# Kernel tuning notes

Hardware: AMD Instinct MI355X
Metric: run time of the kernel (lower is better)

Reference implementation:

```python
import jax, jax.numpy as jnp
import numpy as np

HID = 256

def setup_inputs() -> dict:
    key = jax.random.key(0)
    ks = jax.random.split(key, 16)
    B, N, DIN, DOUT = 256, 1024, 64, 128
    def lin(k, fin, fout):
        kw, kb = jax.random.split(k)
        s = 1.0 / np.sqrt(fin)
        W = jax.random.uniform(kw, (fin, fout), jnp.float32, -s, s)
        b = jax.random.uniform(kb, (fout,), jnp.float32, -s, s)
        return W, b
    x = jax.random.normal(ks[0], (B, N, DIN), jnp.float32)
    mask = jax.random.randint(ks[1], (B, N), 0, 2) > 0
    pw1, pb1 = lin(ks[2], DIN, HID)
    pw2, pb2 = lin(ks[3], HID, HID)
    pw3, pb3 = lin(ks[4], HID, HID)
    rw1, rb1 = lin(ks[5], HID, HID)
    rw2, rb2 = lin(ks[6], HID, HID)
    rw3, rb3 = lin(ks[7], HID, DOUT)
    return dict(x=x, mask=mask, pw1=pw1, pb1=pb1, pw2=pw2, pb2=pb2, pw3=pw3, pb3=pb3,
                rw1=rw1, rb1=rb1, rw2=rw2, rb2=rb2, rw3=rw3, rb3=rb3)

def reference(x, mask, pw1, pb1, pw2, pb2, pw3, pb3, rw1, rb1, rw2, rb2, rw3, rb3):
    # x: [B, N, din], mask: [B, N] bool
    # phi per element (padding elements are zeroed before the pool, matching
    # the torch pack/pad pipeline which only runs phi on valid elements)
    h = jax.nn.relu(jnp.einsum('bnd,dh->bnh', x, pw1) + pb1)
    h = jax.nn.relu(jnp.einsum('bnh,hk->bnk', h, pw2) + pb2)
    h = jnp.einsum('bnh,hk->bnk', h, pw3) + pb3
    m = mask.astype(x.dtype)[..., None]                  # [B, N, 1]
    pooled = jnp.sum(h * m, axis=1)                      # [B, 256]
    o = jax.nn.relu(pooled @ rw1 + rb1)
    o = jax.nn.relu(o @ rw2 + rb2)
    o = o @ rw3 + rb3                                    # [B, dout]
    # rows with zero valid elements get exactly 0 (torch leaves res at 0.0)
    valid = jnp.any(mask, axis=1, keepdims=True)
    return jnp.where(valid, o, jnp.zeros((), dtype=o.dtype))
```

## Files before the change

kernel.cpp:

```cpp
#include <hip/hip_runtime.h>

namespace {
constexpr int NB = 256, NN = 1024, DIN = 64, HID = 256, DOUT = 128;
constexpr int MT = 64;

typedef __attribute__((ext_vector_type(8))) short bf16x8;
typedef __attribute__((ext_vector_type(4))) float f32x4;

__device__ inline unsigned short f2bf(float f) {
    union { float f; unsigned u; } v; v.f = f;
    unsigned r = v.u + 0x7FFF + ((v.u >> 16) & 1);
    return (unsigned short)(r >> 16);
}

__device__ inline float4 dotseg(const float* __restrict__ buf, const float* __restrict__ W,
                                int c, int s) {
    const float4* W4 = (const float4*)W;
    float4 acc = make_float4(0.f, 0.f, 0.f, 0.f);
#pragma unroll 8
    for (int i = 0; i < 32; ++i) {
        int k = s * 32 + i;
        float bk = buf[k];
        float4 w = W4[(size_t)k * 64 + c];
        acc.x = fmaf(bk, w.x, acc.x);
        acc.y = fmaf(bk, w.y, acc.y);
        acc.z = fmaf(bk, w.z, acc.z);
        acc.w = fmaf(bk, w.w, acc.w);
    }
    return acc;
}

__launch_bounds__(512, 1)
__global__ void deepset(const float* __restrict__ x, const int* __restrict__ mask,
                        const float* __restrict__ pw1, const float* __restrict__ pb1,
                        const float* __restrict__ pw2, const float* __restrict__ pb2,
                        const float* __restrict__ pw3, const float* __restrict__ pb3,
                        const float* __restrict__ rw1, const float* __restrict__ rb1,
                        const float* __restrict__ rw2, const float* __restrict__ rb2,
                        const float* __restrict__ rw3, const float* __restrict__ rb3,
                        float* __restrict__ out)
{
    __shared__ unsigned short xs[2][MT * 64];
    __shared__ unsigned short h1s[2][MT * 256];
    __shared__ short vlist[NN];
    __shared__ float pooledS[HID];
    __shared__ float part[8][HID];
    __shared__ float bufB[HID], bufC[HID];
    __shared__ int cnt_s;

    const int b = blockIdx.x, t = threadIdx.x;
    const int lane = t & 63, wq = t >> 6;
    const int quad = lane >> 4, l15 = lane & 15;

    if (t == 0) cnt_s = 0;
    __syncthreads();
#pragma unroll
    for (int h = 0; h < 2; ++h) {
        int idx = h * 512 + t;
        int m = mask[b * NN + idx] != 0;
        unsigned long long bal = __ballot(m);
        int pos = __popcll(bal & ((1ULL << lane) - 1ULL));
        int wbase = 0;
        if (lane == 0) wbase = atomicAdd(&cnt_s, (int)__popcll(bal));
        wbase = __shfl(wbase, 0, 64);
        if (m) vlist[wbase + pos] = (short)idx;
    }

    uint4 w1f[2][2], w2f[8][2];
    float bias1[2], bias2[2];
#pragma unroll
    for (int j = 0; j < 2; ++j) {
        const int col = wq * 32 + j * 16 + l15;
        bias1[j] = pb1[col]; bias2[j] = pb2[col];
#pragma unroll
        for (int kk = 0; kk < 2; ++kk) {
            unsigned short tmp[8];
#pragma unroll
            for (int jj = 0; jj < 8; ++jj)
                tmp[jj] = f2bf(pw1[(size_t)(kk * 32 + quad * 8 + jj) * HID + col]);
            w1f[kk][j] = *(const uint4*)tmp;
        }
#pragma unroll
        for (int kk = 0; kk < 8; ++kk) {
            unsigned short tmp[8];
#pragma unroll
            for (int jj = 0; jj < 8; ++jj)
                tmp[jj] = f2bf(pw2[(size_t)(kk * 32 + quad * 8 + jj) * HID + col]);
            w2f[kk][j] = *(const uint4*)tmp;
        }
    }

    __syncthreads();
    const int cnt = cnt_s;
    const int T = (cnt + MT - 1) / MT;

    float pool[2] = {0.f, 0.f};
    const float* xb = x + (size_t)b * NN * DIN;
    const int gr = t >> 3, seg8 = t & 7;
    const int xoff = gr * 64 + ((seg8 ^ (gr & 7)) << 3);

    if (T > 0) {
        float4 a0 = make_float4(0.f,0.f,0.f,0.f), a1 = a0;
        if (gr < min(MT, cnt)) {
            const float4* p = (const float4*)(xb + (size_t)vlist[gr] * DIN + seg8 * 8);
            a0 = p[0]; a1 = p[1];
        }
        unsigned short tmp[8] = {f2bf(a0.x),f2bf(a0.y),f2bf(a0.z),f2bf(a0.w),
                                 f2bf(a1.x),f2bf(a1.y),f2bf(a1.z),f2bf(a1.w)};
        *(uint4*)&xs[0][xoff] = *(const uint4*)tmp;
    }

    int p = 0;
    for (int i = 0; i <= T; ++i, p ^= 1) {
        __syncthreads();
        const bool doL1 = (i < T);
        const bool hn = ((i + 1) * MT) < cnt;

        float4 n0 = make_float4(0.f,0.f,0.f,0.f), n1 = n0;
        if (doL1 && gr < cnt - (i + 1) * MT) {
            const float4* pp = (const float4*)(xb + (size_t)vlist[(i + 1) * MT + gr] * DIN + seg8 * 8);
            n0 = pp[0]; n1 = pp[1];
        }

        if (doL1) {
            f32x4 acc[4][2];
#pragma unroll
            for (int f = 0; f < 4; ++f)
#pragma unroll
                for (int j = 0; j < 2; ++j) acc[f][j] = (f32x4){0.f,0.f,0.f,0.f};
#pragma unroll
            for (int kk = 0; kk < 2; ++kk) {
                bf16x8 a[4];
#pragma unroll
                for (int f = 0; f < 4; ++f)
                    a[f] = *(const bf16x8*)&xs[p][(f*16 + l15)*64 + (((kk*4 + quad) ^ (l15 & 7)) << 3)];
#pragma unroll
                for (int j = 0; j < 2; ++j) {
                    bf16x8 bw = __builtin_bit_cast(bf16x8, w1f[kk][j]);
#pragma unroll
                    for (int f = 0; f < 4; ++f)
                        acc[f][j] = __builtin_amdgcn_mfma_f32_16x16x32_bf16(a[f], bw, acc[f][j], 0, 0, 0);
                }
            }
#pragma unroll
            for (int f = 0; f < 4; ++f)
#pragma unroll
                for (int j = 0; j < 2; ++j) {
                    int col = wq * 32 + j * 16 + l15, kb = col >> 3, cl = col & 7;
#pragma unroll
                    for (int r = 0; r < 4; ++r) {
                        int row = f * 16 + quad * 4 + r;
                        float h = fmaxf(acc[f][j][r] + bias1[j], 0.f);
                        h1s[p][row * 256 + ((kb ^ (row & 7)) << 3) + cl] = f2bf(h);
                    }
                }
        }

        if (i > 0) {
            const int basep = (i - 1) * MT;
            f32x4 acc2[4][2];
#pragma unroll
            for (int f = 0; f < 4; ++f)
#pragma unroll
                for (int j = 0; j < 2; ++j) acc2[f][j] = (f32x4){0.f,0.f,0.f,0.f};
#pragma unroll
            for (int kk = 0; kk < 8; ++kk) {
                bf16x8 a[4];
#pragma unroll
                for (int f = 0; f < 4; ++f)
                    a[f] = *(const bf16x8*)&h1s[p ^ 1][(f*16 + l15)*256 + (((kk*4 + quad) ^ (l15 & 7)) << 3)];
#pragma unroll
                for (int j = 0; j < 2; ++j) {
                    bf16x8 bw = __builtin_bit_cast(bf16x8, w2f[kk][j]);
#pragma unroll
                    for (int f = 0; f < 4; ++f)
                        acc2[f][j] = __builtin_amdgcn_mfma_f32_16x16x32_bf16(a[f], bw, acc2[f][j], 0, 0, 0);
                }
            }
#pragma unroll
            for (int f = 0; f < 4; ++f)
#pragma unroll
                for (int r = 0; r < 4; ++r) {
                    bool v = (basep + f * 16 + quad * 4 + r) < cnt;
#pragma unroll
                    for (int j = 0; j < 2; ++j) {
                        float h = fmaxf(acc2[f][j][r] + bias2[j], 0.f);
                        pool[j] += v ? h : 0.f;
                    }
                }
        }

        if (hn) {
            unsigned short tmp[8] = {f2bf(n0.x),f2bf(n0.y),f2bf(n0.z),f2bf(n0.w),
                                     f2bf(n1.x),f2bf(n1.y),f2bf(n1.z),f2bf(n1.w)};
            *(uint4*)&xs[p ^ 1][xoff] = *(const uint4*)tmp;
        }
    }

#pragma unroll
    for (int j = 0; j < 2; ++j) {
        float v = pool[j];
        v += __shfl_xor(v, 16, 64);
        v += __shfl_xor(v, 32, 64);
        if (quad == 0) pooledS[wq * 32 + j * 16 + l15] = v;
    }
    __syncthreads();

    const int c = t & 63, s = t >> 6;
    {
        float4 pt = dotseg(pooledS, pw3, c, s);
        ((float4*)part[s])[c] = pt;
        __syncthreads();
        if (t < HID) {
            float v = (float)cnt * pb3[t];
#pragma unroll
            for (int g = 0; g < 8; ++g) v += part[g][t];
            bufB[t] = v;
        }
        __syncthreads();
    }
    {
        float4 pt = dotseg(bufB, rw1, c, s);
        ((float4*)part[s])[c] = pt;
        __syncthreads();
        if (t < HID) {
            float v = rb1[t];
#pragma unroll
            for (int g = 0; g < 8; ++g) v += part[g][t];
            bufC[t] = fmaxf(v, 0.f);
        }
        __syncthreads();
    }
    {
        float4 pt = dotseg(bufC, rw2, c, s);
        ((float4*)part[s])[c] = pt;
        __syncthreads();
        if (t < HID) {
            float v = rb2[t];
#pragma unroll
            for (int g = 0; g < 8; ++g) v += part[g][t];
            bufB[t] = fmaxf(v, 0.f);
        }
        __syncthreads();
    }
    {
        const int c4 = t & 31, s4 = t >> 5;
        const float4* W4 = (const float4*)rw3;
        float4 acc = make_float4(0.f, 0.f, 0.f, 0.f);
#pragma unroll 8
        for (int i = 0; i < 16; ++i) {
            int k = s4 * 16 + i;
            float bk = bufB[k];
            float4 w = W4[(size_t)k * 32 + c4];
            acc.x = fmaf(bk, w.x, acc.x);
            acc.y = fmaf(bk, w.y, acc.y);
            acc.z = fmaf(bk, w.z, acc.z);
            acc.w = fmaf(bk, w.w, acc.w);
        }
        float* part2 = &part[0][0];
        ((float4*)(part2 + s4 * DOUT))[c4] = acc;
        __syncthreads();
        if (t < DOUT) {
            float v = rb3[t];
#pragma unroll
            for (int g = 0; g < 16; ++g) v += part2[g * DOUT + t];
            out[b * DOUT + t] = (cnt > 0) ? v : 0.f;
        }
    }
}
}

extern "C" void kernel_launch(void* const* d_in, const int* in_sizes, int n_in,
                              void* d_out, int out_size, void* d_ws, size_t ws_size,
                              hipStream_t stream) {
    const float* x    = (const float*)d_in[0];
    const int*   mask = (const int*)  d_in[1];
    const float* pw1  = (const float*)d_in[2];
    const float* pb1  = (const float*)d_in[3];
    const float* pw2  = (const float*)d_in[4];
    const float* pb2  = (const float*)d_in[5];
    const float* pw3  = (const float*)d_in[6];
    const float* pb3  = (const float*)d_in[7];
    const float* rw1  = (const float*)d_in[8];
    const float* rb1  = (const float*)d_in[9];
    const float* rw2  = (const float*)d_in[10];
    const float* rb2  = (const float*)d_in[11];
    const float* rw3  = (const float*)d_in[12];
    const float* rb3  = (const float*)d_in[13];
    float* out = (float*)d_out;
    (void)d_ws; (void)ws_size;

    deepset<<<dim3(NB), dim3(512), 0, stream>>>(x, mask, pw1, pb1, pw2, pb2,
                                                pw3, pb3, rw1, rb1, rw2, rb2, rw3, rb3, out);
}
```

Baseline: 147.7 us.

## Swap MFMA operands for transposed output and interleave layer-1/layer-2 MFMAs

Swaps the A/B operands of the MFMA calls so each lane holds 4 consecutive hidden columns for one row. This allows packed 8-byte bf16 stores of the layer-1 activations into LDS, and float4 bias loads, in place of scalar 2-byte stores. It also merges the layer-1 and layer-2 MFMA loops into one k-loop so the independent MFMAs interleave, and changes the pooling reduction to shuffles across the 16 lanes. The cost is more live accumulator registers at once, which may raise register pressure.

```diff
diff --git a/kernel.cpp b/kernel.cpp
--- a/kernel.cpp
+++ b/kernel.cpp
@@ -51,6 +51,8 @@
     const int b = blockIdx.x, t = threadIdx.x;
     const int lane = t & 63, wq = t >> 6;
     const int quad = lane >> 4, l15 = lane & 15;
+    const int sw = l15 & 7;
+    const int cb0 = wq * 32 + quad * 4;
 
     if (t == 0) cnt_s = 0;
     __syncthreads();
@@ -67,11 +69,12 @@
     }
 
     uint4 w1f[2][2], w2f[8][2];
-    float bias1[2], bias2[2];
+    float4 bias1v[2], bias2v[2];
 #pragma unroll
     for (int j = 0; j < 2; ++j) {
         const int col = wq * 32 + j * 16 + l15;
-        bias1[j] = pb1[col]; bias2[j] = pb2[col];
+        bias1v[j] = *(const float4*)&pb1[cb0 + j * 16];
+        bias2v[j] = *(const float4*)&pb2[cb0 + j * 16];
 #pragma unroll
         for (int kk = 0; kk < 2; ++kk) {
             unsigned short tmp[8];
@@ -94,7 +97,7 @@
     const int cnt = cnt_s;
     const int T = (cnt + MT - 1) / MT;
 
-    float pool[2] = {0.f, 0.f};
+    float pool[2][4] = {{0.f,0.f,0.f,0.f},{0.f,0.f,0.f,0.f}};
     const float* xb = x + (size_t)b * NN * DIN;
     const int gr = t >> 3, seg8 = t & 7;
     const int xoff = gr * 64 + ((seg8 ^ (gr & 7)) << 3);
@@ -114,6 +117,7 @@
     for (int i = 0; i <= T; ++i, p ^= 1) {
         __syncthreads();
         const bool doL1 = (i < T);
+        const bool doL2 = (i > 0);
         const bool hn = ((i + 1) * MT) < cnt;
 
         float4 n0 = make_float4(0.f,0.f,0.f,0.f), n1 = n0;
@@ -122,71 +126,77 @@
             n0 = pp[0]; n1 = pp[1];
         }
 
-        if (doL1) {
-            f32x4 acc[4][2];
-#pragma unroll
-            for (int f = 0; f < 4; ++f)
-#pragma unroll
-                for (int j = 0; j < 2; ++j) acc[f][j] = (f32x4){0.f,0.f,0.f,0.f};
-#pragma unroll
-            for (int kk = 0; kk < 2; ++kk) {
-                bf16x8 a[4];
+        f32x4 acc[2][4], acc2[2][4];
+#pragma unroll
+        for (int j = 0; j < 2; ++j)
+#pragma unroll
+            for (int f = 0; f < 4; ++f) {
+                acc[j][f]  = (f32x4){0.f,0.f,0.f,0.f};
+                acc2[j][f] = (f32x4){0.f,0.f,0.f,0.f};
+            }
+
+#pragma unroll
+        for (int kk = 0; kk < 8; ++kk) {
+            bf16x8 aL2[4], aL1[4];
+            if (doL2) {
 #pragma unroll
                 for (int f = 0; f < 4; ++f)
-                    a[f] = *(const bf16x8*)&xs[p][(f*16 + l15)*64 + (((kk*4 + quad) ^ (l15 & 7)) << 3)];
+                    aL2[f] = *(const bf16x8*)&h1s[p ^ 1][(f*16 + l15)*256 + (((kk*4 + quad) ^ sw) << 3)];
+            }
+            if (doL1 && kk < 2) {
+#pragma unroll
+                for (int f = 0; f < 4; ++f)
+                    aL1[f] = *(const bf16x8*)&xs[p][(f*16 + l15)*64 + (((kk*4 + quad) ^ sw) << 3)];
 #pragma unroll
                 for (int j = 0; j < 2; ++j) {
                     bf16x8 bw = __builtin_bit_cast(bf16x8, w1f[kk][j]);
 #pragma unroll
                     for (int f = 0; f < 4; ++f)
-                        acc[f][j] = __builtin_amdgcn_mfma_f32_16x16x32_bf16(a[f], bw, acc[f][j], 0, 0, 0);
+                        acc[j][f] = __builtin_amdgcn_mfma_f32_16x16x32_bf16(bw, aL1[f], acc[j][f], 0, 0, 0);
                 }
             }
-#pragma unroll
-            for (int f = 0; f < 4; ++f)
+            if (doL2) {
 #pragma unroll
                 for (int j = 0; j < 2; ++j) {
-                    int col = wq * 32 + j * 16 + l15, kb = col >> 3, cl = col & 7;
-#pragma unroll
-                    for (int r = 0; r < 4; ++r) {
-                        int row = f * 16 + quad * 4 + r;
-                        float h = fmaxf(acc[f][j][r] + bias1[j], 0.f);
-                        h1s[p][row * 256 + ((kb ^ (row & 7)) << 3) + cl] = f2bf(h);
-                    }
+                    bf16x8 bw2 = __builtin_bit_cast(bf16x8, w2f[kk][j]);
+#pragma unroll
+                    for (int f = 0; f < 4; ++f)
+                        acc2[j][f] = __builtin_amdgcn_mfma_f32_16x16x32_bf16(bw2, aL2[f], acc2[j][f], 0, 0, 0);
                 }
-        }
-
-        if (i > 0) {
+            }
+        }
+
+        if (doL1) {
+#pragma unroll
+            for (int j = 0; j < 2; ++j) {
+                int kb = wq * 4 + j * 2 + (quad >> 1);
+#pragma unroll
+                for (int f = 0; f < 4; ++f) {
+                    int row = f * 16 + l15;
+                    unsigned lo = (unsigned)f2bf(fmaxf(acc[j][f][0] + bias1v[j].x, 0.f))
+                                | ((unsigned)f2bf(fmaxf(acc[j][f][1] + bias1v[j].y, 0.f)) << 16);
+                    unsigned hi = (unsigned)f2bf(fmaxf(acc[j][f][2] + bias1v[j].z, 0.f))
+                                | ((unsigned)f2bf(fmaxf(acc[j][f][3] + bias1v[j].w, 0.f)) << 16);
+                    *(uint2*)&h1s[p][row * 256 + ((kb ^ sw) << 3) + ((quad & 1) << 2)] = make_uint2(lo, hi);
+                }
+            }
+        }
+
+        if (doL2) {
             const int basep = (i - 1) * MT;
-            f32x4 acc2[4][2];
-#pragma unroll
-            for (int f = 0; f < 4; ++f)
-#pragma unroll
-                for (int j = 0; j < 2; ++j) acc2[f][j] = (f32x4){0.f,0.f,0.f,0.f};
-#pragma unroll
-            for (int kk = 0; kk < 8; ++kk) {
-                bf16x8 a[4];
-#pragma unroll
-                for (int f = 0; f < 4; ++f)
-                    a[f] = *(const bf16x8*)&h1s[p ^ 1][(f*16 + l15)*256 + (((kk*4 + quad) ^ (l15 & 7)) << 3)];
-#pragma unroll
-                for (int j = 0; j < 2; ++j) {
-                    bf16x8 bw = __builtin_bit_cast(bf16x8, w2f[kk][j]);
-#pragma unroll
-                    for (int f = 0; f < 4; ++f)
-                        acc2[f][j] = __builtin_amdgcn_mfma_f32_16x16x32_bf16(a[f], bw, acc2[f][j], 0, 0, 0);
-                }
-            }
-#pragma unroll
-            for (int f = 0; f < 4; ++f)
-#pragma unroll
-                for (int r = 0; r < 4; ++r) {
-                    bool v = (basep + f * 16 + quad * 4 + r) < cnt;
-#pragma unroll
-                    for (int j = 0; j < 2; ++j) {
-                        float h = fmaxf(acc2[f][j][r] + bias2[j], 0.f);
-                        pool[j] += v ? h : 0.f;
-                    }
+#pragma unroll
+            for (int j = 0; j < 2; ++j)
+#pragma unroll
+                for (int f = 0; f < 4; ++f) {
+                    bool vf = (basep + f * 16 + l15) < cnt;
+                    float h0 = fmaxf(acc2[j][f][0] + bias2v[j].x, 0.f);
+                    float h1 = fmaxf(acc2[j][f][1] + bias2v[j].y, 0.f);
+                    float h2 = fmaxf(acc2[j][f][2] + bias2v[j].z, 0.f);
+                    float h3 = fmaxf(acc2[j][f][3] + bias2v[j].w, 0.f);
+                    pool[j][0] += vf ? h0 : 0.f;
+                    pool[j][1] += vf ? h1 : 0.f;
+                    pool[j][2] += vf ? h2 : 0.f;
+                    pool[j][3] += vf ? h3 : 0.f;
                 }
         }
 
@@ -198,11 +208,22 @@
     }
 
 #pragma unroll
-    for (int j = 0; j < 2; ++j) {
-        float v = pool[j];
-        v += __shfl_xor(v, 16, 64);
-        v += __shfl_xor(v, 32, 64);
-        if (quad == 0) pooledS[wq * 32 + j * 16 + l15] = v;
+    for (int j = 0; j < 2; ++j)
+#pragma unroll
+        for (int r = 0; r < 4; ++r) {
+            float v = pool[j][r];
+            v += __shfl_xor(v, 1, 64);
+            v += __shfl_xor(v, 2, 64);
+            v += __shfl_xor(v, 4, 64);
+            v += __shfl_xor(v, 8, 64);
+            pool[j][r] = v;
+        }
+    if (l15 == 0) {
+#pragma unroll
+        for (int j = 0; j < 2; ++j) {
+            float4 pv = make_float4(pool[j][0], pool[j][1], pool[j][2], pool[j][3]);
+            *(float4*)&pooledS[cb0 + j * 16] = pv;
+        }
     }
     __syncthreads();
 
```

Result: no change. 146.3 us (-1.0%).
